# Kernel tuning notes

Hardware: AMD Instinct MI355X
Metric: run time of the kernel (lower is better)

Reference implementation:

```python
import jax, jax.numpy as jnp
import numpy as np

B, T, D = 8, 4096, 256
GATE_MIN, GATE_MAX = 0.01, 0.99


def setup_inputs() -> dict:
    key = jax.random.key(0)
    ks = jax.random.split(key, 8)
    inp = {
        "x_re": jax.random.normal(ks[0], (B, T, D), jnp.float32),
        "x_im": jax.random.normal(ks[1], (B, T, D), jnp.float32),
        "s0_re": jnp.zeros((B, D), jnp.float32),
        "s0_im": jnp.zeros((B, D), jnp.float32),
        "decay_re": jax.random.normal(ks[2], (D,), jnp.float32),
        "decay_im": 0.1 * jax.random.normal(ks[3], (D,), jnp.float32),
        "Wm": 0.02 * jax.random.normal(ks[4], (2 * D, 2 * D), jnp.float32)
              + jnp.eye(2 * D, dtype=jnp.float32),  # eye_ init on diag blocks
        "bm": jnp.zeros((2 * D,), jnp.float32),
        "Wo": 0.02 * jax.random.normal(ks[5], (2 * D, 2 * D), jnp.float32),
        "bo": jnp.zeros((2 * D,), jnp.float32),
        "Wg": 0.02 * jax.random.normal(ks[6], (D, 2 * D), jnp.float32),
        "bg": jnp.zeros((D,), jnp.float32),
    }
    return inp


def reference(x_re, x_im, s0_re, s0_im, decay_re, decay_im,
              Wm, bm, Wo, bo, Wg, bg):
    # decay = sigmoid(decay_re) + i*decay_im
    dr = jax.nn.sigmoid(decay_re)
    di = decay_im

    # scan over time: inputs as [T, B, D]
    xs = (jnp.swapaxes(x_re, 0, 1), jnp.swapaxes(x_im, 0, 1))

    def step(carry, xt):
        s_re, s_im = carry
        xr, xi = xt                                   # [B, D]
        x_cat = jnp.concatenate([xr, xi], axis=-1)    # [B, 2D]
        x_in = x_cat @ Wm.T + bm
        ur, ui = jnp.split(x_in, 2, axis=-1)
        # complex mul-add: new_state = prev_state * decay + update
        ns_re = s_re * dr - s_im * di + ur
        ns_im = s_re * di + s_im * dr + ui
        s_cat = jnp.concatenate([ns_re, ns_im], axis=-1)  # [B, 2D]
        source = s_cat @ Wo.T + bo                        # [B, 2D] (re|im)
        gate = jnp.clip(jax.nn.sigmoid(s_cat @ Wg.T + bg), GATE_MIN, GATE_MAX)
        y = jnp.concatenate([source, gate], axis=-1)      # [B, 3D]
        return (ns_re, ns_im), y

    _, ys = jax.lax.scan(step, (s0_re, s0_im), xs)        # [T, B, 3D]
    return jnp.swapaxes(ys, 0, 1)                          # [B, T, 3D] = [src_re|src_im|gate]
```

## Files before the change

### kernel.cpp

```cpp
#include <hip/hip_runtime.h>
#include <hip/hip_bf16.h>
#include <cstdint>
#include <cstddef>


typedef __bf16 bf16;
typedef __bf16 bf16x8 __attribute__((ext_vector_type(8)));
typedef float floatx4 __attribute__((ext_vector_type(4)));

#define NB 8
#define NT 4096
#define ND 256
#define BT (NB * NT)
#define TWOD 512
#define CHUNK 32
#define NCHUNK (NT / CHUNK)

static __device__ __forceinline__ float sigmoidf_(float x) {
  return 1.0f / (1.0f + __expf(-x));
}

static __device__ __forceinline__ void async_copy16(const void* g, void* l) {
  __builtin_amdgcn_global_load_lds(
      (__attribute__((address_space(1))) void*)g,
      (__attribute__((address_space(3))) void*)l, 16, 0, 0);
}

union U32BF2 { unsigned int u; __bf16 h[2]; };

__global__ void k_prep(const float* __restrict__ Wm,
                       const float* __restrict__ bm,
                       const float* __restrict__ Wo,
                       const float* __restrict__ Wg,
                       const float* __restrict__ bo,
                       const float* __restrict__ bg,
                       bf16* __restrict__ Wm_b,
                       bf16* __restrict__ Wc_b,
                       float* __restrict__ bm_p,
                       float* __restrict__ bc) {
  const int i = blockIdx.x * 256 + threadIdx.x;
  {
    const int r = i >> 9, c = i & 511;
    const int sr = (r >> 1) + (r & 1) * 256;
    Wm_b[i] = (bf16)Wm[sr * 512 + c];
  }
  {
    const int r = i >> 9, c = i & 511;
    const int sc = (c >> 1) + (c & 1) * 256;
    Wc_b[i] = (bf16)Wo[r * 512 + sc];
    if (i < 131072) Wc_b[262144 + i] = (bf16)Wg[r * 512 + sc];
  }
  if (i < 512) { bm_p[i] = bm[(i >> 1) + (i & 1) * 256]; bc[i] = bo[i]; }
  if (i < 256) bc[512 + i] = bg[i];
}

__global__ __launch_bounds__(256) void gemm1(
    const float* __restrict__ xre, const float* __restrict__ xim,
    const bf16* __restrict__ Bw, const float* __restrict__ bias,
    bf16* __restrict__ Cu,
    const float* __restrict__ decay_re, const float* __restrict__ decay_im,
    float2* __restrict__ Fc) {
  __shared__ __align__(16) bf16 smem[128 * 128];
  bf16* As = smem;
  bf16* Bs = smem + 128 * 64;
  bf16* Us = smem;
  const int tid = threadIdx.x;
  const int wave = tid >> 6;
  const int lane = tid & 63;
  const int quad = lane >> 4;
  const int l16 = lane & 15;
  const int bid = blockIdx.x;
  const int nb = (bid & 7) * 128 + (bid >> 3);
  const int m0 = (nb >> 2) * 128;
  const int n0 = (nb & 3) * 128;
  const int wm = (wave >> 1) * 64;
  const int wn = (wave & 1) * 64;
  const int srow = lane >> 3;
  const int schunk = (lane & 7) ^ (srow & 7);
  const int ar = tid >> 3;
  const int sg = tid & 7;

  floatx4 acc[4][4];
#pragma unroll
  for (int i = 0; i < 4; ++i)
#pragma unroll
    for (int j = 0; j < 4; ++j) acc[i][j] = (floatx4)0.0f;

  for (int k0 = 0; k0 < 512; k0 += 64) {
    const float* xs = (k0 < 256) ? xre : xim;
    const int xcol = k0 & 255;
    __syncthreads();
#pragma unroll
    for (int i = 0; i < 4; ++i) {
      const int seg = wave * 4 + i;
      const int row = seg * 8 + srow;
      async_copy16(Bw + (size_t)(n0 + row) * 512 + k0 + schunk * 8, Bs + seg * 512);
    }
#pragma unroll
    for (int it = 0; it < 4; ++it) {
      const int r = ar + 32 * it;
      const int cg = sg ^ (r & 7);
      const float* src = xs + (size_t)(m0 + r) * 256 + xcol + cg * 8;
      const float4 f0 = *(const float4*)(src);
      const float4 f1 = *(const float4*)(src + 4);
      bf16x8 v;
      v[0] = (bf16)f0.x; v[1] = (bf16)f0.y; v[2] = (bf16)f0.z; v[3] = (bf16)f0.w;
      v[4] = (bf16)f1.x; v[5] = (bf16)f1.y; v[6] = (bf16)f1.z; v[7] = (bf16)f1.w;
      *(bf16x8*)(As + r * 64 + sg * 8) = v;
    }
    __syncthreads();

#pragma unroll
    for (int s = 0; s < 2; ++s) {
      bf16x8 af[4], bfr[4];
#pragma unroll
      for (int mi = 0; mi < 4; ++mi) {
        const int row = wm + mi * 16 + l16;
        const int ch = ((s << 2) | quad) ^ (l16 & 7);
        af[mi] = *(const bf16x8*)(As + row * 64 + ch * 8);
      }
#pragma unroll
      for (int ni = 0; ni < 4; ++ni) {
        const int row = wn + ni * 16 + l16;
        const int ch = ((s << 2) | quad) ^ (l16 & 7);
        bfr[ni] = *(const bf16x8*)(Bs + row * 64 + ch * 8);
      }
#pragma unroll
      for (int mi = 0; mi < 4; ++mi)
#pragma unroll
        for (int ni = 0; ni < 4; ++ni)
          acc[mi][ni] = __builtin_amdgcn_mfma_f32_16x16x32_bf16(
              af[mi], bfr[ni], acc[mi][ni], 0, 0, 0);
    }
  }

  __syncthreads();
#pragma unroll
  for (int mi = 0; mi < 4; ++mi) {
    const int rloc = wm + mi * 16 + quad * 4;
#pragma unroll
    for (int ni = 0; ni < 4; ++ni) {
      const int cloc = wn + ni * 16 + l16;
      const float bb = bias[n0 + cloc];
#pragma unroll
      for (int r = 0; r < 4; ++r)
        Us[(rloc + r) * 128 + cloc] = (bf16)(acc[mi][ni][r] + bb);
    }
  }
  __syncthreads();
  {
    bf16* dst = Cu + (size_t)m0 * TWOD + n0;
#pragma unroll
    for (int i = 0; i < 8; ++i) {
      const int e = i * 256 + tid;
      const int row = e >> 4, ch = e & 15;
      *(bf16x8*)(dst + (size_t)row * TWOD + ch * 8) =
          *(const bf16x8*)(Us + row * 128 + ch * 8);
    }
  }
  {
    const int sc = tid >> 6;
    const int dd = tid & 63;
    const int d = (n0 >> 1) + dd;
    const float drr = sigmoidf_(decay_re[d]);
    const float dii = decay_im[d];
    float sr = 0.f, si = 0.f;
    const unsigned int* Up = (const unsigned int*)(Us + (sc * 32) * 128 + 2 * dd);
#pragma unroll 4
    for (int j = 0; j < 32; ++j) {
      U32BF2 cv; cv.u = Up[j * 64];
      const float ur = (float)cv.h[0];
      const float ui = (float)cv.h[1];
      const float nr = sr * drr - si * dii + ur;
      const float ni2 = sr * dii + si * drr + ui;
      sr = nr; si = ni2;
    }
    const int bidx = m0 >> 12;
    const int cchunk = ((m0 & 4095) >> 5) + sc;
    const int o = (bidx * NCHUNK + cchunk) * ND + d;
    Fc[o] = make_float2(sr, si);
  }
}

__global__ void k_scan2(const float2* __restrict__ Fc,
                        const float* __restrict__ s0_re,
                        const float* __restrict__ s0_im,
                        const float* __restrict__ decay_re,
                        const float* __restrict__ decay_im,
                        float2* __restrict__ Icx) {
  const int c = threadIdx.x;
  const int d = blockIdx.x;
  const int b = blockIdx.y;
  const float drr = sigmoidf_(decay_re[d]);
  const float dii = decay_im[d];
  float wr = drr, wi = dii;
#pragma unroll
  for (int i = 0; i < 5; ++i) {
    const float nr = wr * wr - wi * wi;
    const float ni = 2.f * wr * wi;
    wr = nr; wi = ni;
  }
  const int o = (b * NCHUNK + c) * ND + d;
  const float2 fv = Fc[o];
  float vr = fv.x, vi = fv.y;
  float ar = 1.f, ai = 0.f;
  __shared__ float lr[128], li[128];
#pragma unroll
  for (int k = 1; k < 128; k <<= 1) {
    lr[c] = vr; li[c] = vi;
    __syncthreads();
    const float tr = (c >= k) ? lr[c - k] : 0.f;
    const float ti = (c >= k) ? li[c - k] : 0.f;
    __syncthreads();
    vr += wr * tr - wi * ti;
    vi += wr * ti + wi * tr;
    if (c & k) {
      const float nar = ar * wr - ai * wi;
      ai = ar * wi + ai * wr;
      ar = nar;
    }
    const float nwr = wr * wr - wi * wi;
    wi = 2.f * wr * wi;
    wr = nwr;
  }
  lr[c] = vr; li[c] = vi;
  __syncthreads();
  float er = (c > 0) ? lr[c - 1] : 0.f;
  float ei = (c > 0) ? li[c - 1] : 0.f;
  const float s0r = s0_re[b * ND + d];
  const float s0i = s0_im[b * ND + d];
  er += ar * s0r - ai * s0i;
  ei += ar * s0i + ai * s0r;
  Icx[o] = make_float2(er, ei);
}

__global__ __launch_bounds__(128) void k_scan_pass3(
    bf16* __restrict__ U,
    const float* __restrict__ decay_re,
    const float* __restrict__ decay_im,
    const float2* __restrict__ Icx) {
  const int t = threadIdx.x;
  const int c = blockIdx.x;
  const int b = blockIdx.y;
  const int d0 = 2 * t;
  const float dr0 = sigmoidf_(decay_re[d0]);
  const float di0 = decay_im[d0];
  const float dr1 = sigmoidf_(decay_re[d0 + 1]);
  const float di1 = decay_im[d0 + 1];
  const int o = (b * NCHUNK + c) * ND + d0;
  const float4 iv = *(const float4*)(&Icx[o]);
  float sr0 = iv.x, si0 = iv.y, sr1 = iv.z, si1 = iv.w;
  uint2* Ur = (uint2*)
      (U + ((size_t)b * NT + (size_t)c * CHUNK) * TWOD + 2 * d0);
#pragma unroll 8
  for (int j = 0; j < CHUNK; ++j) {
    uint2 cv = Ur[(size_t)j * (TWOD / 4)];
    U32BF2 a0, a1; a0.u = cv.x; a1.u = cv.y;
    const float ur0 = (float)a0.h[0], ui0 = (float)a0.h[1];
    const float ur1 = (float)a1.h[0], ui1 = (float)a1.h[1];
    const float nr0 = sr0 * dr0 - si0 * di0 + ur0;
    const float ni0 = sr0 * di0 + si0 * dr0 + ui0;
    const float nr1 = sr1 * dr1 - si1 * di1 + ur1;
    const float ni1 = sr1 * di1 + si1 * dr1 + ui1;
    sr0 = nr0; si0 = ni0; sr1 = nr1; si1 = ni1;
    a0.h[0] = (bf16)nr0; a0.h[1] = (bf16)ni0;
    a1.h[0] = (bf16)nr1; a1.h[1] = (bf16)ni1;
    cv.x = a0.u; cv.y = a1.u;
    Ur[(size_t)j * (TWOD / 4)] = cv;
  }
}

__global__ __launch_bounds__(256) void gemm2(
    const bf16* __restrict__ A, const bf16* __restrict__ Bw,
    const float* __restrict__ bias, float* __restrict__ C) {
  __shared__ __align__(16) bf16 As[128 * 64];
  __shared__ __align__(16) bf16 Bs[64 * 64];
  const int tid = threadIdx.x;
  const int wave = tid >> 6;
  const int lane = tid & 63;
  const int quad = lane >> 4;
  const int l16 = lane & 15;
  const int bid = blockIdx.x;
  const int nb = (bid & 7) * 384 + (bid >> 3);
  const int m0 = (nb / 12) * 128;
  const int n0 = (nb % 12) * 64;
  const int wm = (wave >> 1) * 64;
  const int wn = (wave & 1) * 32;
  const int srow = lane >> 3;
  const int schunk = (lane & 7) ^ (srow & 7);

  floatx4 acc[4][2];
#pragma unroll
  for (int i = 0; i < 4; ++i)
#pragma unroll
    for (int j = 0; j < 2; ++j) acc[i][j] = (floatx4)0.0f;

  for (int k0 = 0; k0 < 512; k0 += 64) {
    __syncthreads();
#pragma unroll
    for (int i = 0; i < 4; ++i) {
      const int seg = wave * 4 + i;
      const int row = seg * 8 + srow;
      async_copy16(A + (size_t)(m0 + row) * 512 + k0 + schunk * 8, As + seg * 512);
    }
#pragma unroll
    for (int i = 0; i < 2; ++i) {
      const int seg = wave * 2 + i;
      const int row = seg * 8 + srow;
      async_copy16(Bw + (size_t)(n0 + row) * 512 + k0 + schunk * 8, Bs + seg * 512);
    }
    __syncthreads();

#pragma unroll
    for (int s = 0; s < 2; ++s) {
      bf16x8 af[4], bfr[2];
#pragma unroll
      for (int mi = 0; mi < 4; ++mi) {
        const int row = wm + mi * 16 + l16;
        const int ch = ((s << 2) | quad) ^ (l16 & 7);
        af[mi] = *(const bf16x8*)(As + row * 64 + ch * 8);
      }
#pragma unroll
      for (int ni = 0; ni < 2; ++ni) {
        const int row = wn + ni * 16 + l16;
        const int ch = ((s << 2) | quad) ^ (l16 & 7);
        bfr[ni] = *(const bf16x8*)(Bs + row * 64 + ch * 8);
      }
#pragma unroll
      for (int mi = 0; mi < 4; ++mi)
#pragma unroll
        for (int ni = 0; ni < 2; ++ni)
          acc[mi][ni] = __builtin_amdgcn_mfma_f32_16x16x32_bf16(
              af[mi], bfr[ni], acc[mi][ni], 0, 0, 0);
    }
  }

#pragma unroll
  for (int mi = 0; mi < 4; ++mi) {
    const int rb = m0 + wm + mi * 16 + quad * 4;
#pragma unroll
    for (int ni = 0; ni < 2; ++ni) {
      const int col = n0 + wn + ni * 16 + l16;
      const float bb = bias[col];
#pragma unroll
      for (int r = 0; r < 4; ++r) {
        float v = acc[mi][ni][r] + bb;
        if (col >= 512) v = fminf(fmaxf(sigmoidf_(v), 0.01f), 0.99f);
        C[(size_t)(rb + r) * 768 + col] = v;
      }
    }
  }
}


extern "C" void kernel_launch(void* const* d_in, const int* in_sizes, int n_in,
                              void* d_out, int out_size, void* d_ws, size_t ws_size,
                              hipStream_t stream) {
  const float* x_re = (const float*)d_in[0];
  const float* x_im = (const float*)d_in[1];
  const float* s0_re = (const float*)d_in[2];
  const float* s0_im = (const float*)d_in[3];
  const float* decay_re = (const float*)d_in[4];
  const float* decay_im = (const float*)d_in[5];
  const float* Wm = (const float*)d_in[6];
  const float* bm = (const float*)d_in[7];
  const float* Wo = (const float*)d_in[8];
  const float* bo = (const float*)d_in[9];
  const float* Wg = (const float*)d_in[10];
  const float* bg = (const float*)d_in[11];

  char* ws = (char*)d_ws;
  const size_t U_OFF = 0;
  const size_t WM_OFF = 33554432;
  const size_t WC_OFF = WM_OFF + 524288;
  const size_t BMP_OFF = WC_OFF + 786432;
  const size_t BC_OFF = BMP_OFF + 4096;
  const size_t FC_OFF = BC_OFF + 4096;
  const size_t IC_OFF = FC_OFF + 2097152;

  bf16* U = (bf16*)(ws + U_OFF);
  bf16* Wm_b = (bf16*)(ws + WM_OFF);
  bf16* Wc_b = (bf16*)(ws + WC_OFF);
  float* bm_p = (float*)(ws + BMP_OFF);
  float* bc = (float*)(ws + BC_OFF);
  float2* Fc = (float2*)(ws + FC_OFF);
  float2* Icx = (float2*)(ws + IC_OFF);

  k_prep<<<dim3(1024), 256, 0, stream>>>(Wm, bm, Wo, Wg, bo, bg,
                                         Wm_b, Wc_b, bm_p, bc);
  gemm1<<<dim3(1024), 256, 0, stream>>>(x_re, x_im, Wm_b, bm_p, U,
                                        decay_re, decay_im, Fc);
  k_scan2<<<dim3(ND, NB), NCHUNK, 0, stream>>>(Fc, s0_re, s0_im,
                                               decay_re, decay_im, Icx);
  k_scan_pass3<<<dim3(NCHUNK, NB), 128, 0, stream>>>(U, decay_re, decay_im, Icx);
  gemm2<<<dim3(3072), 256, 0, stream>>>(U, Wc_b, bc, (float*)d_out);
}
```

Measured before the change: 246.4 us.

## Double-buffer shared-memory tiles in both GEMM kernels to overlap loads with MFMA

Both GEMM kernels now use two shared-memory buffers for the A and B tiles. The next K-slice is prefetched with async global-to-LDS copies and register loads while MFMAs run on the current slice, which cuts one barrier per iteration. gemm1 holds the fp32 x values in registers and converts and writes them to the alternate buffer after the compute step. This doubles LDS use (64KB in gemm1, 48KB in gemm2), which may lower occupancy and adds register pressure.

```diff
diff --git a/kernel.cpp b/kernel.cpp
--- a/kernel.cpp
+++ b/kernel.cpp
@@ -60,9 +60,7 @@
     bf16* __restrict__ Cu,
     const float* __restrict__ decay_re, const float* __restrict__ decay_im,
     float2* __restrict__ Fc) {
-  __shared__ __align__(16) bf16 smem[128 * 128];
-  bf16* As = smem;
-  bf16* Bs = smem + 128 * 64;
+  __shared__ __align__(16) bf16 smem[32768];
   bf16* Us = smem;
   const int tid = threadIdx.x;
   const int wave = tid >> 6;
@@ -86,30 +84,55 @@
 #pragma unroll
     for (int j = 0; j < 4; ++j) acc[i][j] = (floatx4)0.0f;
 
-  for (int k0 = 0; k0 < 512; k0 += 64) {
-    const float* xs = (k0 < 256) ? xre : xim;
-    const int xcol = k0 & 255;
-    __syncthreads();
-#pragma unroll
-    for (int i = 0; i < 4; ++i) {
-      const int seg = wave * 4 + i;
-      const int row = seg * 8 + srow;
-      async_copy16(Bw + (size_t)(n0 + row) * 512 + k0 + schunk * 8, Bs + seg * 512);
-    }
-#pragma unroll
-    for (int it = 0; it < 4; ++it) {
-      const int r = ar + 32 * it;
-      const int cg = sg ^ (r & 7);
-      const float* src = xs + (size_t)(m0 + r) * 256 + xcol + cg * 8;
-      const float4 f0 = *(const float4*)(src);
-      const float4 f1 = *(const float4*)(src + 4);
-      bf16x8 v;
-      v[0] = (bf16)f0.x; v[1] = (bf16)f0.y; v[2] = (bf16)f0.z; v[3] = (bf16)f0.w;
-      v[4] = (bf16)f1.x; v[5] = (bf16)f1.y; v[6] = (bf16)f1.z; v[7] = (bf16)f1.w;
-      *(bf16x8*)(As + r * 64 + sg * 8) = v;
-    }
-    __syncthreads();
-
+  float4 a0[4], a1[4];
+
+#define STAGE_B(buf, k0)                                                       \
+  _Pragma("unroll")                                                            \
+  for (int i = 0; i < 4; ++i) {                                                \
+    const int seg = wave * 4 + i;                                              \
+    const int row = seg * 8 + srow;                                            \
+    async_copy16(Bw + (size_t)(n0 + row) * 512 + (k0) + schunk * 8,            \
+                 smem + 16384 + (buf) * 8192 + seg * 512);                     \
+  }
+#define LOAD_A(k0)                                                             \
+  {                                                                            \
+    const float* xs = ((k0) < 256) ? xre : xim;                                \
+    const int xcol = (k0) & 255;                                               \
+    _Pragma("unroll")                                                          \
+    for (int it = 0; it < 4; ++it) {                                           \
+      const int r = ar + 32 * it;                                              \
+      const int cg = sg ^ (r & 7);                                             \
+      const float* src = xs + (size_t)(m0 + r) * 256 + xcol + cg * 8;          \
+      a0[it] = *(const float4*)(src);                                          \
+      a1[it] = *(const float4*)(src + 4);                                      \
+    }                                                                          \
+  }
+#define WRITE_A(buf)                                                           \
+  _Pragma("unroll")                                                            \
+  for (int it = 0; it < 4; ++it) {                                             \
+    const int r = ar + 32 * it;                                                \
+    bf16x8 v;                                                                  \
+    v[0] = (bf16)a0[it].x; v[1] = (bf16)a0[it].y;                              \
+    v[2] = (bf16)a0[it].z; v[3] = (bf16)a0[it].w;                              \
+    v[4] = (bf16)a1[it].x; v[5] = (bf16)a1[it].y;                              \
+    v[6] = (bf16)a1[it].z; v[7] = (bf16)a1[it].w;                              \
+    *(bf16x8*)(smem + (buf) * 8192 + r * 64 + sg * 8) = v;                     \
+  }
+
+  STAGE_B(0, 0)
+  LOAD_A(0)
+  WRITE_A(0)
+  __syncthreads();
+
+  int cur = 0;
+  for (int t = 0; t < 8; ++t) {
+    const bool hn = (t < 7);
+    if (hn) {
+      STAGE_B(cur ^ 1, (t + 1) * 64)
+      LOAD_A((t + 1) * 64)
+    }
+    const bf16* Asc = smem + cur * 8192;
+    const bf16* Bsc = smem + 16384 + cur * 8192;
 #pragma unroll
     for (int s = 0; s < 2; ++s) {
       bf16x8 af[4], bfr[4];
@@ -117,13 +140,13 @@
       for (int mi = 0; mi < 4; ++mi) {
         const int row = wm + mi * 16 + l16;
         const int ch = ((s << 2) | quad) ^ (l16 & 7);
-        af[mi] = *(const bf16x8*)(As + row * 64 + ch * 8);
+        af[mi] = *(const bf16x8*)(Asc + row * 64 + ch * 8);
       }
 #pragma unroll
       for (int ni = 0; ni < 4; ++ni) {
         const int row = wn + ni * 16 + l16;
         const int ch = ((s << 2) | quad) ^ (l16 & 7);
-        bfr[ni] = *(const bf16x8*)(Bs + row * 64 + ch * 8);
+        bfr[ni] = *(const bf16x8*)(Bsc + row * 64 + ch * 8);
       }
 #pragma unroll
       for (int mi = 0; mi < 4; ++mi)
@@ -132,9 +155,14 @@
           acc[mi][ni] = __builtin_amdgcn_mfma_f32_16x16x32_bf16(
               af[mi], bfr[ni], acc[mi][ni], 0, 0, 0);
     }
-  }
-
-  __syncthreads();
+    if (hn) WRITE_A(cur ^ 1)
+    __syncthreads();
+    cur ^= 1;
+  }
+#undef STAGE_B
+#undef LOAD_A
+#undef WRITE_A
+
 #pragma unroll
   for (int mi = 0; mi < 4; ++mi) {
     const int rloc = wm + mi * 16 + quad * 4;
@@ -273,8 +301,8 @@
 __global__ __launch_bounds__(256) void gemm2(
     const bf16* __restrict__ A, const bf16* __restrict__ Bw,
     const float* __restrict__ bias, float* __restrict__ C) {
-  __shared__ __align__(16) bf16 As[128 * 64];
-  __shared__ __align__(16) bf16 Bs[64 * 64];
+  __shared__ __align__(16) bf16 As[2][128 * 64];
+  __shared__ __align__(16) bf16 Bs[2][64 * 64];
   const int tid = threadIdx.x;
   const int wave = tid >> 6;
   const int lane = tid & 63;
@@ -295,22 +323,28 @@
 #pragma unroll
     for (int j = 0; j < 2; ++j) acc[i][j] = (floatx4)0.0f;
 
-  for (int k0 = 0; k0 < 512; k0 += 64) {
-    __syncthreads();
-#pragma unroll
-    for (int i = 0; i < 4; ++i) {
-      const int seg = wave * 4 + i;
-      const int row = seg * 8 + srow;
-      async_copy16(A + (size_t)(m0 + row) * 512 + k0 + schunk * 8, As + seg * 512);
-    }
-#pragma unroll
-    for (int i = 0; i < 2; ++i) {
-      const int seg = wave * 2 + i;
-      const int row = seg * 8 + srow;
-      async_copy16(Bw + (size_t)(n0 + row) * 512 + k0 + schunk * 8, Bs + seg * 512);
-    }
-    __syncthreads();
-
+#define STAGE(buf, k0)                                                         \
+  _Pragma("unroll")                                                            \
+  for (int i = 0; i < 4; ++i) {                                                \
+    const int seg = wave * 4 + i;                                              \
+    const int row = seg * 8 + srow;                                            \
+    async_copy16(A + (size_t)(m0 + row) * 512 + (k0) + schunk * 8,             \
+                 &As[buf][seg * 512]);                                         \
+  }                                                                            \
+  _Pragma("unroll")                                                            \
+  for (int i = 0; i < 2; ++i) {                                                \
+    const int seg = wave * 2 + i;                                              \
+    const int row = seg * 8 + srow;                                            \
+    async_copy16(Bw + (size_t)(n0 + row) * 512 + (k0) + schunk * 8,            \
+                 &Bs[buf][seg * 512]);                                         \
+  }
+
+  STAGE(0, 0)
+  __syncthreads();
+
+  int cur = 0;
+  for (int t = 0; t < 8; ++t) {
+    if (t < 7) { STAGE(cur ^ 1, (t + 1) * 64) }
 #pragma unroll
     for (int s = 0; s < 2; ++s) {
       bf16x8 af[4], bfr[2];
@@ -318,13 +352,13 @@
       for (int mi = 0; mi < 4; ++mi) {
         const int row = wm + mi * 16 + l16;
         const int ch = ((s << 2) | quad) ^ (l16 & 7);
-        af[mi] = *(const bf16x8*)(As + row * 64 + ch * 8);
+        af[mi] = *(const bf16x8*)(&As[cur][row * 64 + ch * 8]);
       }
 #pragma unroll
       for (int ni = 0; ni < 2; ++ni) {
         const int row = wn + ni * 16 + l16;
         const int ch = ((s << 2) | quad) ^ (l16 & 7);
-        bfr[ni] = *(const bf16x8*)(Bs + row * 64 + ch * 8);
+        bfr[ni] = *(const bf16x8*)(&Bs[cur][row * 64 + ch * 8]);
       }
 #pragma unroll
       for (int mi = 0; mi < 4; ++mi)
@@ -333,7 +367,10 @@
           acc[mi][ni] = __builtin_amdgcn_mfma_f32_16x16x32_bf16(
               af[mi], bfr[ni], acc[mi][ni], 0, 0, 0);
     }
-  }
+    __syncthreads();
+    cur ^= 1;
+  }
+#undef STAGE
 
 #pragma unroll
   for (int mi = 0; mi < 4; ++mi) {
```

New measurement: 255.7 us. +3.8%, slower.
